# Kernel optimization log

Measured on AMD Instinct MI355X. Metric: run time of the kernel, lower is better.

The kernel has to match this reference:

```python
import jax, jax.numpy as jnp
import numpy as np

D = 256            # number of graph nodes (example.size(3))
K1 = D // 2        # topkpool1 k
K2 = D // 4        # topkpool2 k
B = 8


def _lrelu(x):
    return jnp.where(x > 0, x, 0.33 * x)


def _e2e(h, wa, ba, wb, bb):
    # h: [B,C,d,d]; wa,wb: [P,C,d] (squeezed (1,d)/(d,1) conv kernels)
    # cnn1: contract over columns j -> [B,P,d]; cnn2: contract over rows i -> [B,P,d]
    a = jnp.einsum('bcij,pcj->bpi', h, wa) + ba[None, :, None]
    b = jnp.einsum('bcij,pci->bpj', h, wb) + bb[None, :, None]
    # cat([a]*d, 3) + cat([b]*d, 2)  ==  broadcast-add
    return a[:, :, :, None] + b[:, :, None, :]


def _gcn(h, g, W, b):
    # h: [B,N,F_in], g: [B,N,N]; faithful to norm_g: g[i,j] / deg[j] (column-normalized
    # because torch broadcasts the [N] degree vector over the LAST dim)
    gb = (g > 0).astype(h.dtype)
    deg = gb.sum(axis=2)                      # [B,N] row sums
    gn = gb / deg[:, None, :]                 # divide column j by deg[j]
    return jnp.einsum('bij,bjf->bif', gn, h) @ W.T + b


def _pool(h, g, s, k):
    # h: [B,N,F], g: [B,N,N], s: [B,N,1] -> top-k nodes by score (descending)
    vals, idx = jax.lax.top_k(s[:, :, 0], k)              # [B,k]
    hn = jnp.take_along_axis(h, idx[:, :, None], axis=1)  # [B,k,F]
    gn = jnp.take_along_axis(g, idx[:, :, None], axis=1)
    gn = jnp.take_along_axis(gn, idx[:, None, :], axis=2) # [B,k,k]
    return hn, gn, vals[:, :, None]


def _readout(h):
    # h: [B,N,F] (node axis = 1); torch ReadOut on [B,F,N,1] max/mean over dim=2
    return jnp.concatenate([h.max(axis=1), h.mean(axis=1)], axis=1)  # [B,2F]


def _forward(x, w1a, b1a, w1b, b1b, w2a, b2a, w2b, b2b, e2n_w, e2n_b,
             a11_w, a11_b, a12_w, a12_b, g1_w, g1_b,
             a21_w, a21_b, a22_w, a22_b,
             d1_w, d1_b, d2_w, d2_b, d3_w, d3_b):
    h = _lrelu(_e2e(x, w1a, b1a, w1b, b1b))         # [B,128,d,d]
    h = _lrelu(_e2e(h, w2a, b2a, w2b, b2b))         # [B,256,d,d]
    # E2N conv (1,d): [B,8,d,1] -> node features [B,d,8]
    nodes = _lrelu(jnp.einsum('bcij,pcj->bpi', h, e2n_w) + e2n_b[None, :, None])
    nodes = jnp.transpose(nodes, (0, 2, 1))          # [B,d,8]
    g0 = x[:, 0]                                     # [B,d,d]

    w = _lrelu(_gcn(nodes, g0, a11_w, a11_b))        # [B,d,1]
    w = jax.nn.sigmoid(_gcn(w, g0, a12_w, a12_b))
    h1, g1, s1 = _pool(nodes, g0, w, K1)             # [B,K1,8], [B,K1,K1], [B,K1,1]
    out = h1 * s1 + h1
    sum1 = _readout(out)                             # [B,16]

    h2 = _gcn(out, g1, g1_w, g1_b)                   # [B,K1,8] (no activation, as in torch)
    w = _lrelu(_gcn(h2, g1, a21_w, a21_b))
    w = jax.nn.sigmoid(_gcn(w, g1, a22_w, a22_b))
    h3, g2, s2 = _pool(h2, g1, w, K2)                # [B,K2,8]
    out2 = h3 * s2 + h3
    sum2 = _readout(out2)                            # [B,16]

    z = sum1 + sum2                                  # [B,16]
    z = _lrelu(z @ d1_w.T + d1_b)                    # dropout = identity (eval mode)
    z = _lrelu(z @ d2_w.T + d2_b)
    return z @ d3_w.T + d3_b                         # [B,1]


def setup_inputs() -> dict:
    key = jax.random.key(0)
    ks = jax.random.split(key, 16)
    f32 = jnp.float32

    def rn(k, shape, scale):
        return jax.random.normal(k, shape, dtype=f32) * scale

    return {
        'x': jax.random.normal(ks[0], (B, 1, D, D), dtype=f32),
        'w1a': rn(ks[1], (128, 1, D), 0.08),  'b1a': jnp.zeros((128,), f32),
        'w1b': rn(ks[2], (128, 1, D), 0.08),  'b1b': jnp.zeros((128,), f32),
        'w2a': rn(ks[3], (256, 128, D), 0.008), 'b2a': jnp.zeros((256,), f32),
        'w2b': rn(ks[4], (256, 128, D), 0.008), 'b2b': jnp.zeros((256,), f32),
        'e2n_w': rn(ks[5], (8, 256, D), 0.005), 'e2n_b': jnp.zeros((8,), f32),
        'a11_w': rn(ks[6], (1, 8), 0.3),  'a11_b': jnp.zeros((1,), f32),
        'a12_w': rn(ks[7], (1, 1), 0.3),  'a12_b': jnp.zeros((1,), f32),
        'g1_w': rn(ks[8], (8, 8), 0.3),   'g1_b': jnp.zeros((8,), f32),
        'a21_w': rn(ks[9], (1, 8), 0.3),  'a21_b': jnp.zeros((1,), f32),
        'a22_w': rn(ks[10], (1, 1), 0.3), 'a22_b': jnp.zeros((1,), f32),
        'd1_w': rn(ks[11], (128, 16), 0.2), 'd1_b': jnp.zeros((128,), f32),
        'd2_w': rn(ks[12], (64, 128), 0.08), 'd2_b': jnp.zeros((64,), f32),
        'd3_w': rn(ks[13], (1, 64), 0.1),  'd3_b': jnp.zeros((1,), f32),
    }


def reference(x, w1a, b1a, w1b, b1b, w2a, b2a, w2b, b2b, e2n_w, e2n_b,
              a11_w, a11_b, a12_w, a12_b, g1_w, g1_b,
              a21_w, a21_b, a22_w, a22_b,
              d1_w, d1_b, d2_w, d2_b, d3_w, d3_b):
    return _forward(x, w1a, b1a, w1b, b1b, w2a, b2a, w2b, b2b, e2n_w, e2n_b,
                    a11_w, a11_b, a12_w, a12_b, g1_w, g1_b,
                    a21_w, a21_b, a22_w, a22_b,
                    d1_w, d1_b, d2_w, d2_b, d3_w, d3_b)
```

## Files before the change

### kernel.cpp

```cpp
#include <hip/hip_runtime.h>

typedef short s16x8 __attribute__((ext_vector_type(8)));
typedef float f32x4 __attribute__((ext_vector_type(4)));
typedef float f32x2 __attribute__((ext_vector_type(2)));

#define TID threadIdx.x

__device__ __forceinline__ float lrelu_f(float x) { return fmaxf(x, 0.33f * x); }

__device__ __forceinline__ unsigned lrelu_pack(float pv, f32x2 q) {
    f32x2 s = q + pv;
    f32x2 m = s * 0.33f;
    f32x2 r = __builtin_elementwise_max(s, m);
    unsigned u;
    asm("v_cvt_pk_bf16_f32 %0, %1, %2" : "=v"(u) : "v"(r.x), "v"(r.y));
    return u;
}
__device__ __forceinline__ unsigned pk_bf16(float a, float b) {
    unsigned u;
    asm("v_cvt_pk_bf16_f32 %0, %1, %2" : "=v"(u) : "v"(a), "v"(b));
    return u;
}

union FragU { s16x8 v; uint4 q; unsigned w[4]; };

__global__ __launch_bounds__(256) void k_convert(
    const float* __restrict__ sa, unsigned short* __restrict__ da, int na4,
    const float* __restrict__ sb, unsigned short* __restrict__ db, int nb4,
    const float* __restrict__ sc, unsigned short* __restrict__ dc, int nc4)
{
    const float* s; unsigned short* d; int n4;
    if (blockIdx.y == 0)      { s = sa; d = da; n4 = na4; }
    else if (blockIdx.y == 1) { s = sb; d = db; n4 = nb4; }
    else                      { s = sc; d = dc; n4 = nc4; }
    const int stride = gridDim.x * 256;
    for (int i = blockIdx.x * 256 + TID; i < n4; i += stride) {
        float4 v = ((const float4*)s)[i];
        ((uint2*)d)[i] = make_uint2(pk_bf16(v.x, v.y), pk_bf16(v.z, v.w));
    }
}

__global__ __launch_bounds__(128) void k_l1(
    const float* __restrict__ x,
    const float* __restrict__ w1a, const float* __restrict__ b1a,
    const float* __restrict__ w1b, const float* __restrict__ b1b,
    float* __restrict__ A1, float* __restrict__ B1)
{
    const int r = blockIdx.x, b = blockIdx.y, v = blockIdx.z;
    const int tid = TID;
    __shared__ float xr[256];
    const float* xb = x + b * 65536;
    if (v == 0) {
        xr[tid]       = xb[r * 256 + tid];
        xr[tid + 128] = xb[r * 256 + tid + 128];
    } else {
        xr[tid]       = xb[tid * 256 + r];
        xr[tid + 128] = xb[(tid + 128) * 256 + r];
    }
    __syncthreads();
    const float* w    = v ? w1b : w1a;
    const float* bias = v ? b1b : b1a;
    float* OUT = v ? B1 : A1;
    float acc = bias[tid];
    const float* wr = w + tid * 256;
    #pragma unroll 4
    for (int q = 0; q < 256; q += 8) {
        float4 a = *(const float4*)(wr + q);
        float4 c = *(const float4*)(wr + q + 4);
        acc += xr[q + 0] * a.x + xr[q + 1] * a.y + xr[q + 2] * a.z + xr[q + 3] * a.w;
        acc += xr[q + 4] * c.x + xr[q + 5] * c.y + xr[q + 6] * c.z + xr[q + 7] * c.w;
    }
    OUT[b * 32768 + tid * 256 + r] = acc;
}

__global__ __launch_bounds__(512) void k_e2e(
    const float* __restrict__ A1, const float* __restrict__ B1,
    const unsigned short* __restrict__ w2aM, const unsigned short* __restrict__ w2bM,
    float* __restrict__ part)
{
    const int rt = blockIdx.x;
    const int s  = blockIdx.y;
    const int bw = blockIdx.z;
    const int b = bw >> 1, which = bw & 1;
    const float* P = (which ? B1 : A1) + b * 32768;
    const float* Q = (which ? A1 : B1) + b * 32768;
    const unsigned short* W = which ? w2bM : w2aM;
    const int c0 = s * 16, r0 = rt * 128;

    __shared__ float Qs[16][256];
    __shared__ float Ps[16][128];

    const int tid = TID;
    {
        const float4* Qg = (const float4*)(Q + c0 * 256);
        float4* Qd = (float4*)&Qs[0][0];
        Qd[tid]       = Qg[tid];
        Qd[tid + 512] = Qg[tid + 512];
        int row = tid >> 5, col = tid & 31;
        *(float4*)&Ps[row][col * 4] = *(const float4*)&P[(c0 + row) * 256 + r0 + col * 4];
    }
    __syncthreads();

    const int wave = tid >> 6, lane = tid & 63, quad = lane >> 4, l16 = lane & 15;
    const int wi = wave & 3, wj = wave >> 2;
    const int pbase = wi * 64, rbase = wj * 64;

    f32x4 acc[4][4] = {};

    const unsigned short* Wrow[4];
    #pragma unroll
    for (int pf = 0; pf < 4; ++pf)
        Wrow[pf] = W + (size_t)(pbase + pf * 16 + l16) * 32768 + c0 * 256 + quad * 8;

    FragU af[2][4];
    f32x2 qp[2][4];
    float pv[4], pvn[4];

    #pragma unroll
    for (int pf = 0; pf < 4; ++pf) af[0][pf].q = *(const uint4*)(Wrow[pf]);
    #pragma unroll
    for (int k = 0; k < 4; ++k) qp[0][k] = *(const f32x2*)&Qs[0][quad * 8 + 2 * k];
    #pragma unroll
    for (int nf = 0; nf < 4; ++nf) pv[nf] = Ps[0][rbase + nf * 16 + l16];

    for (int c = 0; c < 16; ++c) {
        #pragma unroll
        for (int q0 = 0; q0 < 8; ++q0) {
            const int cur = q0 & 1, nxt = cur ^ 1;
            const int cn = (q0 == 7) ? c + 1 : c;
            const int qn = (q0 + 1) & 7;
            if (cn < 16) {
                #pragma unroll
                for (int pf = 0; pf < 4; ++pf)
                    af[nxt][pf].q = *(const uint4*)(Wrow[pf] + cn * 256 + qn * 32);
                #pragma unroll
                for (int k = 0; k < 4; ++k)
                    qp[nxt][k] = *(const f32x2*)&Qs[cn][qn * 32 + quad * 8 + 2 * k];
            }
            if (q0 == 4 && c + 1 < 16) {
                #pragma unroll
                for (int nf = 0; nf < 4; ++nf) pvn[nf] = Ps[c + 1][rbase + nf * 16 + l16];
            }
            #pragma unroll
            for (int nf = 0; nf < 4; ++nf) {
                FragU hb;
                hb.w[0] = lrelu_pack(pv[nf], qp[cur][0]);
                hb.w[1] = lrelu_pack(pv[nf], qp[cur][1]);
                hb.w[2] = lrelu_pack(pv[nf], qp[cur][2]);
                hb.w[3] = lrelu_pack(pv[nf], qp[cur][3]);
                #pragma unroll
                for (int pf = 0; pf < 4; ++pf)
                    acc[pf][nf] = __builtin_amdgcn_mfma_f32_16x16x32_bf16(af[cur][pf].v, hb.v, acc[pf][nf], 0, 0, 0);
            }
            if (q0 == 7) {
                #pragma unroll
                for (int nf = 0; nf < 4; ++nf) pv[nf] = pvn[nf];
            }
        }
    }
    float* pb = part + (size_t)(s * 16 + bw) * 65536;
    #pragma unroll
    for (int pf = 0; pf < 4; ++pf)
        #pragma unroll
        for (int nf = 0; nf < 4; ++nf)
            #pragma unroll
            for (int t = 0; t < 4; ++t) {
                int p = pbase + pf * 16 + quad * 4 + t;
                int r = r0 + rbase + nf * 16 + l16;
                pb[p * 256 + r] = acc[pf][nf][t];
            }
}

__global__ __launch_bounds__(256) void k_red(
    const float* __restrict__ part,
    const float* __restrict__ b2a, const float* __restrict__ b2b,
    float* __restrict__ A2, float* __restrict__ B2)
{
    const int bw = blockIdx.y; const int b = bw >> 1, which = bw & 1;
    const int idx = blockIdx.x * 256 + TID;
    const float4* pp = (const float4*)part;
    float4 acc = make_float4(0.f, 0.f, 0.f, 0.f);
    #pragma unroll
    for (int s = 0; s < 8; ++s) {
        float4 v = pp[(size_t)(s * 16 + bw) * 16384 + idx];
        acc.x += v.x; acc.y += v.y; acc.z += v.z; acc.w += v.w;
    }
    const int p = idx >> 6;
    const float bias = (which ? b2b : b2a)[p];
    acc.x += bias; acc.y += bias; acc.z += bias; acc.w += bias;
    float* OUT = (which ? B2 : A2) + b * 65536;
    ((float4*)OUT)[idx] = acc;
}

__global__ __launch_bounds__(256) void k_e2n(
    const float* __restrict__ A2, const float* __restrict__ B2,
    const unsigned short* __restrict__ e2nw,
    float* __restrict__ nodes_raw)
{
    const int it = blockIdx.x, b = blockIdx.y, sn = blockIdx.z;
    const int tid = TID, wave = tid >> 6, lane = tid & 63, quad = lane >> 4, l16 = lane & 15;
    const int i0 = it * 16;
    const int c0 = sn * 32 + wave * 8;
    const float* Ab = A2 + b * 65536;
    const float* Bb = B2 + b * 65536;
    const float* Brow0 = Bb + c0 * 256 + quad * 8;
    const unsigned short* Wrow0 = e2nw + (size_t)l16 * 65536 + c0 * 256 + quad * 8;

    f32x4 acc = {};
    FragU af[2];
    f32x2 qp[2][4];
    float pv, pvn;

    if (l16 < 8) af[0].q = *(const uint4*)(Wrow0);
    else         af[0].q = make_uint4(0u, 0u, 0u, 0u);
    #pragma unroll
    for (int k = 0; k < 4; ++k) qp[0][k] = *(const f32x2*)(Brow0 + 2 * k);
    pv = Ab[c0 * 256 + i0 + l16];

    for (int cc = 0; cc < 8; ++cc) {
        #pragma unroll
        for (int q0 = 0; q0 < 8; ++q0) {
            const int cur = q0 & 1, nxt = cur ^ 1;
            const int cn = (q0 == 7) ? cc + 1 : cc;
            const int qn = (q0 + 1) & 7;
            if (cn < 8) {
                if (l16 < 8) af[nxt].q = *(const uint4*)(Wrow0 + cn * 256 + qn * 32);
                else         af[nxt].q = make_uint4(0u, 0u, 0u, 0u);
                #pragma unroll
                for (int k = 0; k < 4; ++k)
                    qp[nxt][k] = *(const f32x2*)(Brow0 + cn * 256 + qn * 32 + 2 * k);
            }
            if (q0 == 4 && cc + 1 < 8) pvn = Ab[(c0 + cc + 1) * 256 + i0 + l16];
            FragU hb;
            hb.w[0] = lrelu_pack(pv, qp[cur][0]);
            hb.w[1] = lrelu_pack(pv, qp[cur][1]);
            hb.w[2] = lrelu_pack(pv, qp[cur][2]);
            hb.w[3] = lrelu_pack(pv, qp[cur][3]);
            acc = __builtin_amdgcn_mfma_f32_16x16x32_bf16(af[cur].v, hb.v, acc, 0, 0, 0);
            if (q0 == 7) pv = pvn;
        }
    }
    __shared__ float red[4][16][16];
    #pragma unroll
    for (int t = 0; t < 4; ++t) red[wave][quad * 4 + t][l16] = acc[t];
    __syncthreads();
    const int row = tid >> 4, col = tid & 15;
    if (row < 8) {
        float ssum = red[0][row][col] + red[1][row][col] + red[2][row][col] + red[3][row][col];
        atomicAdd(&nodes_raw[b * 2048 + (i0 + col) * 8 + row], ssum);
    }
}

__global__ __launch_bounds__(256) void k_adj(
    const float* __restrict__ x,
    unsigned long long* __restrict__ adjw, float* __restrict__ rdegw)
{
    const int b = blockIdx.y;
    const int tid = TID, wave = tid >> 6, lane = tid & 63;
    const int rbase = blockIdx.x * 32 + wave * 8;
    for (int rr = 0; rr < 8; ++rr) {
        const int row = rbase + rr;
        int d = 0;
        unsigned long long w[4];
        #pragma unroll
        for (int k = 0; k < 4; ++k) {
            float v = x[b * 65536 + row * 256 + k * 64 + lane];
            w[k] = __ballot(v > 0.0f);
            d += __popcll(w[k]);
        }
        if (lane == 0) {
            #pragma unroll
            for (int k = 0; k < 4; ++k) adjw[(b * 256 + row) * 4 + k] = w[k];
            rdegw[b * 256 + row] = d ? 1.0f / (float)d : 0.0f;
        }
    }
}

__global__ __launch_bounds__(256) void k_tail(
    const unsigned long long* __restrict__ adjw, const float* __restrict__ rdegw,
    const float* __restrict__ nodes_raw, const float* __restrict__ e2n_b,
    const float* __restrict__ a11_w, const float* __restrict__ a11_b,
    const float* __restrict__ a12_w, const float* __restrict__ a12_b,
    const float* __restrict__ g1_w,  const float* __restrict__ g1_b,
    const float* __restrict__ a21_w, const float* __restrict__ a21_b,
    const float* __restrict__ a22_w, const float* __restrict__ a22_b,
    const float* __restrict__ d1_w,  const float* __restrict__ d1_b,
    const float* __restrict__ d2_w,  const float* __restrict__ d2_b,
    const float* __restrict__ d3_w,  const float* __restrict__ d3_b,
    float* __restrict__ out)
{
    const int b = blockIdx.x;
    const int tid = TID;

    __shared__ unsigned long long adj[256][4];
    __shared__ float nod[256][8];
    __shared__ float rdeg[256];
    __shared__ float md[256];
    __shared__ float w1s[256];
    __shared__ float w2s[256];
    __shared__ int   selflag[256];
    __shared__ int   selidx[128];
    __shared__ float s1v[128];
    __shared__ float out1[128][8];
    __shared__ float aggL[128][8];
    __shared__ float h2L[128][8];
    __shared__ unsigned long long adj1[128][2];
    __shared__ float rdeg1[128];
    __shared__ float tA[128];
    __shared__ float w1t[128];
    __shared__ float w2t[128];
    __shared__ int   sel2flag[128];
    __shared__ int   sel2idx[64];
    __shared__ float s2v[64];
    __shared__ float out2[64][8];
    __shared__ float r1[16], r2[16], zz[16];
    __shared__ float z1[128];
    __shared__ float z2[64];

    if (tid < 128) { selidx[tid] = 0; s1v[tid] = 0.0f; }
    if (tid < 64)  { sel2idx[tid] = 0; s2v[tid] = 0.0f; }

    {
        #pragma unroll
        for (int k = 0; k < 4; ++k) adj[tid][k] = adjw[(b * 256 + tid) * 4 + k];
        rdeg[tid] = rdegw[b * 256 + tid];
        for (int f = 0; f < 8; ++f)
            nod[tid][f] = lrelu_f(nodes_raw[b * 2048 + tid * 8 + f] + e2n_b[f]);
    }
    __syncthreads();
    {
        float s = 0.0f;
        for (int f = 0; f < 8; ++f) s += nod[tid][f] * a11_w[f];
        md[tid] = s * rdeg[tid];
    }
    __syncthreads();
    {
        float s = 0.0f;
        for (int k = 0; k < 4; ++k) {
            unsigned long long m = adj[tid][k];
            while (m) { int j = __builtin_ctzll(m); m &= m - 1; s += md[k * 64 + j]; }
        }
        w1s[tid] = lrelu_f(s + a11_b[0]);
    }
    __syncthreads();
    md[tid] = w1s[tid] * a12_w[0] * rdeg[tid];
    __syncthreads();
    {
        float s = 0.0f;
        for (int k = 0; k < 4; ++k) {
            unsigned long long m = adj[tid][k];
            while (m) { int j = __builtin_ctzll(m); m &= m - 1; s += md[k * 64 + j]; }
        }
        w2s[tid] = 1.0f / (1.0f + expf(-(s + a12_b[0])));
    }
    __syncthreads();
    {
        const float my = w2s[tid];
        int cnt = 0;
        for (int j = 0; j < 256; ++j) {
            float o = w2s[j];
            cnt += (o > my) || (o == my && j < tid);
        }
        selflag[tid] = (cnt < 128) ? 1 : 0;
    }
    __syncthreads();
    if (selflag[tid]) {
        int pos = 0;
        for (int j = 0; j < tid; ++j) pos += selflag[j];
        if (pos < 128) { selidx[pos] = tid; s1v[pos] = w2s[tid]; }
    }
    __syncthreads();
    for (int k = tid; k < 1024; k += 256) {
        int t = k >> 3, f = k & 7;
        out1[t][f] = nod[selidx[t]][f] * (1.0f + s1v[t]);
    }
    __syncthreads();
    if (tid < 16) {
        int f = tid & 7;
        if (tid < 8) {
            float mx = -INFINITY;
            for (int t = 0; t < 128; ++t) mx = fmaxf(mx, out1[t][f]);
            r1[tid] = mx;
        } else {
            float s = 0.0f;
            for (int t = 0; t < 128; ++t) s += out1[t][f];
            r1[tid] = s * (1.0f / 128.0f);
        }
    }
    if (tid < 128) {
        unsigned long long wds[2] = {0ull, 0ull};
        const int gi = selidx[tid];
        for (int u = 0; u < 128; ++u) {
            const int gj = selidx[u];
            unsigned long long bit = (adj[gi][gj >> 6] >> (gj & 63)) & 1ull;
            wds[u >> 6] |= bit << (u & 63);
        }
        adj1[tid][0] = wds[0]; adj1[tid][1] = wds[1];
        int d = __popcll(wds[0]) + __popcll(wds[1]);
        rdeg1[tid] = d ? 1.0f / (float)d : 0.0f;
    }
    __syncthreads();
    {
        const int t = tid >> 1, f0 = (tid & 1) * 4;
        float a0 = 0, a1 = 0, a2 = 0, a3 = 0;
        for (int k = 0; k < 2; ++k) {
            unsigned long long m = adj1[t][k];
            while (m) {
                int u = __builtin_ctzll(m); m &= m - 1;
                int uu = k * 64 + u;
                float rr = rdeg1[uu];
                a0 += out1[uu][f0 + 0] * rr;
                a1 += out1[uu][f0 + 1] * rr;
                a2 += out1[uu][f0 + 2] * rr;
                a3 += out1[uu][f0 + 3] * rr;
            }
        }
        aggL[t][f0 + 0] = a0; aggL[t][f0 + 1] = a1; aggL[t][f0 + 2] = a2; aggL[t][f0 + 3] = a3;
    }
    __syncthreads();
    for (int k = tid; k < 1024; k += 256) {
        int t = k >> 3, fo = k & 7;
        float s = g1_b[fo];
        for (int f = 0; f < 8; ++f) s += aggL[t][f] * g1_w[fo * 8 + f];
        h2L[t][fo] = s;
    }
    __syncthreads();
    if (tid < 128) {
        float s = 0.0f;
        for (int f = 0; f < 8; ++f) s += h2L[tid][f] * a21_w[f];
        tA[tid] = s * rdeg1[tid];
    }
    __syncthreads();
    if (tid < 128) {
        float s = 0.0f;
        for (int k = 0; k < 2; ++k) {
            unsigned long long m = adj1[tid][k];
            while (m) { int u = __builtin_ctzll(m); m &= m - 1; s += tA[k * 64 + u]; }
        }
        w1t[tid] = lrelu_f(s + a21_b[0]);
    }
    __syncthreads();
    if (tid < 128) tA[tid] = w1t[tid] * a22_w[0] * rdeg1[tid];
    __syncthreads();
    if (tid < 128) {
        float s = 0.0f;
        for (int k = 0; k < 2; ++k) {
            unsigned long long m = adj1[tid][k];
            while (m) { int u = __builtin_ctzll(m); m &= m - 1; s += tA[k * 64 + u]; }
        }
        w2t[tid] = 1.0f / (1.0f + expf(-(s + a22_b[0])));
    }
    __syncthreads();
    if (tid < 128) {
        const float my = w2t[tid];
        int cnt = 0;
        for (int u = 0; u < 128; ++u) {
            float o = w2t[u];
            cnt += (o > my) || (o == my && u < tid);
        }
        sel2flag[tid] = (cnt < 64) ? 1 : 0;
    }
    __syncthreads();
    if (tid < 128 && sel2flag[tid]) {
        int pos = 0;
        for (int u = 0; u < tid; ++u) pos += sel2flag[u];
        if (pos < 64) { sel2idx[pos] = tid; s2v[pos] = w2t[tid]; }
    }
    __syncthreads();
    for (int k = tid; k < 512; k += 256) {
        int u = k >> 3, f = k & 7;
        out2[u][f] = h2L[sel2idx[u]][f] * (1.0f + s2v[u]);
    }
    __syncthreads();
    if (tid < 16) {
        int f = tid & 7;
        if (tid < 8) {
            float mx = -INFINITY;
            for (int t = 0; t < 64; ++t) mx = fmaxf(mx, out2[t][f]);
            r2[tid] = mx;
        } else {
            float s = 0.0f;
            for (int t = 0; t < 64; ++t) s += out2[t][f];
            r2[tid] = s * (1.0f / 64.0f);
        }
    }
    __syncthreads();
    if (tid < 16) zz[tid] = r1[tid] + r2[tid];
    __syncthreads();
    if (tid < 128) {
        float s = d1_b[tid];
        for (int k = 0; k < 16; ++k) s += zz[k] * d1_w[tid * 16 + k];
        z1[tid] = lrelu_f(s);
    }
    __syncthreads();
    if (tid < 64) {
        float s = d2_b[tid];
        for (int k = 0; k < 128; ++k) s += z1[k] * d2_w[tid * 128 + k];
        z2[tid] = lrelu_f(s);
    }
    __syncthreads();
    if (tid == 0) {
        float s = d3_b[0];
        for (int k = 0; k < 64; ++k) s += z2[k] * d3_w[k];
        out[b] = s;
    }
}

extern "C" void kernel_launch(void* const* d_in, const int* in_sizes, int n_in,
                              void* d_out, int out_size, void* d_ws, size_t ws_size,
                              hipStream_t stream) {
    const float* x     = (const float*)d_in[0];
    const float* w1a   = (const float*)d_in[1];
    const float* b1a   = (const float*)d_in[2];
    const float* w1b   = (const float*)d_in[3];
    const float* b1b   = (const float*)d_in[4];
    const float* w2a   = (const float*)d_in[5];
    const float* b2a   = (const float*)d_in[6];
    const float* w2b   = (const float*)d_in[7];
    const float* b2b   = (const float*)d_in[8];
    const float* e2nw  = (const float*)d_in[9];

    float* ws        = (float*)d_ws;
    float* A1        = ws;
    float* B1        = ws + 262144;
    float* A2        = ws + 524288;
    float* B2        = ws + 1048576;
    float* nodes_raw = ws + 1572864;
    float* rdegw     = ws + 1589248;
    unsigned long long* adjw = (unsigned long long*)(ws + 1597440);
    float* part      = ws + 1613824;
    unsigned short* w2aM  = (unsigned short*)(ws + 10002432);
    unsigned short* w2bM  = w2aM + 8388608;
    unsigned short* e2nwM = w2bM + 8388608;

    k_convert<<<dim3(512, 3), 256, 0, stream>>>(
        w2a, w2aM, 8388608 / 4,
        w2b, w2bM, 8388608 / 4,
        e2nw, e2nwM, 524288 / 4);
    hipMemsetAsync(nodes_raw, 0, 16384 * sizeof(float), stream);
    k_l1<<<dim3(256, 8, 2), 128, 0, stream>>>(x, w1a, b1a, w1b, b1b, A1, B1);
    k_adj<<<dim3(8, 8), 256, 0, stream>>>(x, adjw, rdegw);
    k_e2e<<<dim3(2, 8, 16), 512, 0, stream>>>(A1, B1, w2aM, w2bM, part);
    k_red<<<dim3(64, 16), 256, 0, stream>>>(part, b2a, b2b, A2, B2);
    k_e2n<<<dim3(16, 8, 8), 256, 0, stream>>>(A2, B2, e2nwM, nodes_raw);
    k_tail<<<dim3(8), 256, 0, stream>>>(adjw, rdegw, nodes_raw, (const float*)d_in[10],
        (const float*)d_in[11], (const float*)d_in[12], (const float*)d_in[13], (const float*)d_in[14],
        (const float*)d_in[15], (const float*)d_in[16], (const float*)d_in[17], (const float*)d_in[18],
        (const float*)d_in[19], (const float*)d_in[20], (const float*)d_in[21], (const float*)d_in[22],
        (const float*)d_in[23], (const float*)d_in[24], (const float*)d_in[25], (const float*)d_in[26],
        (float*)d_out);
}
```

Baseline: 438.6 us.

## Fuse split-K reduction into e2e via atomics and share weights across batch pairs

The e2e layer-2 kernel now handles two batch elements per block, so each loaded bf16 weight fragment feeds MFMAs for both batches, halving weight traffic per output. Partial sums over the channel split go straight into A2/B2 with float atomicAdd instead of a partial buffer plus a separate reduction kernel. The bias is folded into the e2n stage, and a single memset zeroes A2/B2/nodes_raw. The explicit software prefetch double-buffering of weight and LDS fragments is dropped. The trade is many global atomics in place of the reduce pass, plus less latency hiding in the inner loops.

```diff
diff --git a/kernel.cpp b/kernel.cpp
--- a/kernel.cpp
+++ b/kernel.cpp
@@ -76,124 +76,99 @@
 __global__ __launch_bounds__(512) void k_e2e(
     const float* __restrict__ A1, const float* __restrict__ B1,
     const unsigned short* __restrict__ w2aM, const unsigned short* __restrict__ w2bM,
-    float* __restrict__ part)
+    float* __restrict__ A2, float* __restrict__ B2)
 {
-    const int rt = blockIdx.x;
-    const int s  = blockIdx.y;
-    const int bw = blockIdx.z;
-    const int b = bw >> 1, which = bw & 1;
-    const float* P = (which ? B1 : A1) + b * 32768;
-    const float* Q = (which ? A1 : B1) + b * 32768;
+    const int which = blockIdx.x & 1, s = blockIdx.x >> 1;
+    const int bp = blockIdx.y;
+    const int rt = blockIdx.z & 3, ks = blockIdx.z >> 2;
+    const int c0 = s * 16 + ks * 8;
+    const int r0 = rt * 64;
     const unsigned short* W = which ? w2bM : w2aM;
-    const int c0 = s * 16, r0 = rt * 128;
-
-    __shared__ float Qs[16][256];
-    __shared__ float Ps[16][128];
+    const float* Pg[2]; const float* Qg[2]; float* OUT[2];
+    #pragma unroll
+    for (int bt = 0; bt < 2; ++bt) {
+        const int b = bp * 2 + bt;
+        Pg[bt]  = (which ? B1 : A1) + b * 32768;
+        Qg[bt]  = (which ? A1 : B1) + b * 32768;
+        OUT[bt] = (which ? B2 : A2) + b * 65536;
+    }
+
+    __shared__ float Qs[2][8][256];
+    __shared__ float Ps[2][8][64];
 
     const int tid = TID;
     {
-        const float4* Qg = (const float4*)(Q + c0 * 256);
-        float4* Qd = (float4*)&Qs[0][0];
-        Qd[tid]       = Qg[tid];
-        Qd[tid + 512] = Qg[tid + 512];
-        int row = tid >> 5, col = tid & 31;
-        *(float4*)&Ps[row][col * 4] = *(const float4*)&P[(c0 + row) * 256 + r0 + col * 4];
+        #pragma unroll
+        for (int k = 0; k < 2; ++k) {
+            int idx = tid + k * 512;
+            int bt = idx >> 9, rem = idx & 511, c = rem >> 6, q4 = rem & 63;
+            *(float4*)&Qs[bt][c][q4 * 4] = *(const float4*)&Qg[bt][(c0 + c) * 256 + q4 * 4];
+        }
+        if (tid < 256) {
+            int bt = tid >> 7, rem = tid & 127, c = rem >> 4, r4 = rem & 15;
+            *(float4*)&Ps[bt][c][r4 * 4] = *(const float4*)&Pg[bt][(c0 + c) * 256 + r0 + r4 * 4];
+        }
     }
     __syncthreads();
 
     const int wave = tid >> 6, lane = tid & 63, quad = lane >> 4, l16 = lane & 15;
     const int wi = wave & 3, wj = wave >> 2;
-    const int pbase = wi * 64, rbase = wj * 64;
-
-    f32x4 acc[4][4] = {};
+    const int pbase = wi * 64, rbase = wj * 32;
+
+    f32x4 acc[2][4][2] = {};
 
     const unsigned short* Wrow[4];
     #pragma unroll
     for (int pf = 0; pf < 4; ++pf)
         Wrow[pf] = W + (size_t)(pbase + pf * 16 + l16) * 32768 + c0 * 256 + quad * 8;
 
-    FragU af[2][4];
-    f32x2 qp[2][4];
-    float pv[4], pvn[4];
-
+    for (int cc = 0; cc < 8; ++cc) {
+        float pv[2][2];
+        #pragma unroll
+        for (int bt = 0; bt < 2; ++bt)
+            #pragma unroll
+            for (int nf = 0; nf < 2; ++nf)
+                pv[bt][nf] = Ps[bt][cc][rbase + nf * 16 + l16];
+        #pragma unroll
+        for (int q0 = 0; q0 < 8; ++q0) {
+            FragU af[4];
+            #pragma unroll
+            for (int pf = 0; pf < 4; ++pf)
+                af[pf].q = *(const uint4*)(Wrow[pf] + cc * 256 + q0 * 32);
+            #pragma unroll
+            for (int bt = 0; bt < 2; ++bt) {
+                const f32x2* qp = (const f32x2*)&Qs[bt][cc][q0 * 32 + quad * 8];
+                #pragma unroll
+                for (int nf = 0; nf < 2; ++nf) {
+                    FragU hb;
+                    hb.w[0] = lrelu_pack(pv[bt][nf], qp[0]);
+                    hb.w[1] = lrelu_pack(pv[bt][nf], qp[1]);
+                    hb.w[2] = lrelu_pack(pv[bt][nf], qp[2]);
+                    hb.w[3] = lrelu_pack(pv[bt][nf], qp[3]);
+                    #pragma unroll
+                    for (int pf = 0; pf < 4; ++pf)
+                        acc[bt][pf][nf] = __builtin_amdgcn_mfma_f32_16x16x32_bf16(af[pf].v, hb.v, acc[bt][pf][nf], 0, 0, 0);
+                }
+            }
+        }
+    }
     #pragma unroll
-    for (int pf = 0; pf < 4; ++pf) af[0][pf].q = *(const uint4*)(Wrow[pf]);
-    #pragma unroll
-    for (int k = 0; k < 4; ++k) qp[0][k] = *(const f32x2*)&Qs[0][quad * 8 + 2 * k];
-    #pragma unroll
-    for (int nf = 0; nf < 4; ++nf) pv[nf] = Ps[0][rbase + nf * 16 + l16];
-
-    for (int c = 0; c < 16; ++c) {
-        #pragma unroll
-        for (int q0 = 0; q0 < 8; ++q0) {
-            const int cur = q0 & 1, nxt = cur ^ 1;
-            const int cn = (q0 == 7) ? c + 1 : c;
-            const int qn = (q0 + 1) & 7;
-            if (cn < 16) {
+    for (int bt = 0; bt < 2; ++bt)
+        #pragma unroll
+        for (int pf = 0; pf < 4; ++pf)
+            #pragma unroll
+            for (int nf = 0; nf < 2; ++nf)
                 #pragma unroll
-                for (int pf = 0; pf < 4; ++pf)
-                    af[nxt][pf].q = *(const uint4*)(Wrow[pf] + cn * 256 + qn * 32);
-                #pragma unroll
-                for (int k = 0; k < 4; ++k)
-                    qp[nxt][k] = *(const f32x2*)&Qs[cn][qn * 32 + quad * 8 + 2 * k];
-            }
-            if (q0 == 4 && c + 1 < 16) {
-                #pragma unroll
-                for (int nf = 0; nf < 4; ++nf) pvn[nf] = Ps[c + 1][rbase + nf * 16 + l16];
-            }
-            #pragma unroll
-            for (int nf = 0; nf < 4; ++nf) {
-                FragU hb;
-                hb.w[0] = lrelu_pack(pv[nf], qp[cur][0]);
-                hb.w[1] = lrelu_pack(pv[nf], qp[cur][1]);
-                hb.w[2] = lrelu_pack(pv[nf], qp[cur][2]);
-                hb.w[3] = lrelu_pack(pv[nf], qp[cur][3]);
-                #pragma unroll
-                for (int pf = 0; pf < 4; ++pf)
-                    acc[pf][nf] = __builtin_amdgcn_mfma_f32_16x16x32_bf16(af[cur][pf].v, hb.v, acc[pf][nf], 0, 0, 0);
-            }
-            if (q0 == 7) {
-                #pragma unroll
-                for (int nf = 0; nf < 4; ++nf) pv[nf] = pvn[nf];
-            }
-        }
-    }
-    float* pb = part + (size_t)(s * 16 + bw) * 65536;
-    #pragma unroll
-    for (int pf = 0; pf < 4; ++pf)
-        #pragma unroll
-        for (int nf = 0; nf < 4; ++nf)
-            #pragma unroll
-            for (int t = 0; t < 4; ++t) {
-                int p = pbase + pf * 16 + quad * 4 + t;
-                int r = r0 + rbase + nf * 16 + l16;
-                pb[p * 256 + r] = acc[pf][nf][t];
-            }
-}
-
-__global__ __launch_bounds__(256) void k_red(
-    const float* __restrict__ part,
-    const float* __restrict__ b2a, const float* __restrict__ b2b,
-    float* __restrict__ A2, float* __restrict__ B2)
-{
-    const int bw = blockIdx.y; const int b = bw >> 1, which = bw & 1;
-    const int idx = blockIdx.x * 256 + TID;
-    const float4* pp = (const float4*)part;
-    float4 acc = make_float4(0.f, 0.f, 0.f, 0.f);
-    #pragma unroll
-    for (int s = 0; s < 8; ++s) {
-        float4 v = pp[(size_t)(s * 16 + bw) * 16384 + idx];
-        acc.x += v.x; acc.y += v.y; acc.z += v.z; acc.w += v.w;
-    }
-    const int p = idx >> 6;
-    const float bias = (which ? b2b : b2a)[p];
-    acc.x += bias; acc.y += bias; acc.z += bias; acc.w += bias;
-    float* OUT = (which ? B2 : A2) + b * 65536;
-    ((float4*)OUT)[idx] = acc;
+                for (int t = 0; t < 4; ++t) {
+                    int p = pbase + pf * 16 + quad * 4 + t;
+                    int r = r0 + rbase + nf * 16 + l16;
+                    atomicAdd(&OUT[bt][p * 256 + r], acc[bt][pf][nf][t]);
+                }
 }
 
 __global__ __launch_bounds__(256) void k_e2n(
     const float* __restrict__ A2, const float* __restrict__ B2,
+    const float* __restrict__ b2a, const float* __restrict__ b2b,
     const unsigned short* __restrict__ e2nw,
     float* __restrict__ nodes_raw)
 {
@@ -207,37 +182,21 @@
     const unsigned short* Wrow0 = e2nw + (size_t)l16 * 65536 + c0 * 256 + quad * 8;
 
     f32x4 acc = {};
-    FragU af[2];
-    f32x2 qp[2][4];
-    float pv, pvn;
-
-    if (l16 < 8) af[0].q = *(const uint4*)(Wrow0);
-    else         af[0].q = make_uint4(0u, 0u, 0u, 0u);
-    #pragma unroll
-    for (int k = 0; k < 4; ++k) qp[0][k] = *(const f32x2*)(Brow0 + 2 * k);
-    pv = Ab[c0 * 256 + i0 + l16];
-
     for (int cc = 0; cc < 8; ++cc) {
+        const int c = c0 + cc;
+        const float pv = Ab[c * 256 + i0 + l16] + b2a[c] + b2b[c];
         #pragma unroll
         for (int q0 = 0; q0 < 8; ++q0) {
-            const int cur = q0 & 1, nxt = cur ^ 1;
-            const int cn = (q0 == 7) ? cc + 1 : cc;
-            const int qn = (q0 + 1) & 7;
-            if (cn < 8) {
-                if (l16 < 8) af[nxt].q = *(const uint4*)(Wrow0 + cn * 256 + qn * 32);
-                else         af[nxt].q = make_uint4(0u, 0u, 0u, 0u);
-                #pragma unroll
-                for (int k = 0; k < 4; ++k)
-                    qp[nxt][k] = *(const f32x2*)(Brow0 + cn * 256 + qn * 32 + 2 * k);
-            }
-            if (q0 == 4 && cc + 1 < 8) pvn = Ab[(c0 + cc + 1) * 256 + i0 + l16];
+            const f32x2* qp = (const f32x2*)(Brow0 + cc * 256 + q0 * 32);
+            FragU a;
+            if (l16 < 8) a.q = *(const uint4*)(Wrow0 + cc * 256 + q0 * 32);
+            else         a.q = make_uint4(0u, 0u, 0u, 0u);
             FragU hb;
-            hb.w[0] = lrelu_pack(pv, qp[cur][0]);
-            hb.w[1] = lrelu_pack(pv, qp[cur][1]);
-            hb.w[2] = lrelu_pack(pv, qp[cur][2]);
-            hb.w[3] = lrelu_pack(pv, qp[cur][3]);
-            acc = __builtin_amdgcn_mfma_f32_16x16x32_bf16(af[cur].v, hb.v, acc, 0, 0, 0);
-            if (q0 == 7) pv = pvn;
+            hb.w[0] = lrelu_pack(pv, qp[0]);
+            hb.w[1] = lrelu_pack(pv, qp[1]);
+            hb.w[2] = lrelu_pack(pv, qp[2]);
+            hb.w[3] = lrelu_pack(pv, qp[3]);
+            acc = __builtin_amdgcn_mfma_f32_16x16x32_bf16(a.v, hb.v, acc, 0, 0, 0);
         }
     }
     __shared__ float red[4][16][16];
@@ -527,22 +486,20 @@
     float* B2        = ws + 1048576;
     float* nodes_raw = ws + 1572864;
     float* rdegw     = ws + 1589248;
-    unsigned long long* adjw = (unsigned long long*)(ws + 1597440);
-    float* part      = ws + 1613824;
-    unsigned short* w2aM  = (unsigned short*)(ws + 10002432);
+    unsigned long long* adjw = (unsigned long long*)(ws + 1591296);
+    unsigned short* w2aM  = (unsigned short*)(ws + 1607680);
     unsigned short* w2bM  = w2aM + 8388608;
     unsigned short* e2nwM = w2bM + 8388608;
 
+    hipMemsetAsync(A2, 0, 1064960 * sizeof(float), stream);
     k_convert<<<dim3(512, 3), 256, 0, stream>>>(
         w2a, w2aM, 8388608 / 4,
         w2b, w2bM, 8388608 / 4,
         e2nw, e2nwM, 524288 / 4);
-    hipMemsetAsync(nodes_raw, 0, 16384 * sizeof(float), stream);
     k_l1<<<dim3(256, 8, 2), 128, 0, stream>>>(x, w1a, b1a, w1b, b1b, A1, B1);
     k_adj<<<dim3(8, 8), 256, 0, stream>>>(x, adjw, rdegw);
-    k_e2e<<<dim3(2, 8, 16), 512, 0, stream>>>(A1, B1, w2aM, w2bM, part);
-    k_red<<<dim3(64, 16), 256, 0, stream>>>(part, b2a, b2b, A2, B2);
-    k_e2n<<<dim3(16, 8, 8), 256, 0, stream>>>(A2, B2, e2nwM, nodes_raw);
+    k_e2e<<<dim3(16, 4, 8), 512, 0, stream>>>(A1, B1, w2aM, w2bM, A2, B2);
+    k_e2n<<<dim3(16, 8, 8), 256, 0, stream>>>(A2, B2, b2a, b2b, e2nwM, nodes_raw);
     k_tail<<<dim3(8), 256, 0, stream>>>(adjw, rdegw, nodes_raw, (const float*)d_in[10],
         (const float*)d_in[11], (const float*)d_in[12], (const float*)d_in[13], (const float*)d_in[14],
         (const float*)d_in[15], (const float*)d_in[16], (const float*)d_in[17], (const float*)d_in[18],
```

New measurement: 472.1 us. 7.6% more time.
